# Kernel optimization log

Hardware: AMD Instinct MI355X
Metric: run time of the kernel (lower is better)

The kernel has to match this reference:

```python
import jax, jax.numpy as jnp
import numpy as np

N, K, D = 32768, 1024, 256
TAU = 1.0          # gumbel-softmax temperature (torch default)
KL_WEIGHT = 1.0    # settings.kl_weight stand-in
EPS = 1e-6


def setup_inputs() -> dict:
    key = jax.random.key(0)
    k1, k2, k3 = jax.random.split(key, 3)
    latents = jax.random.normal(k1, (N, D), dtype=jnp.float32)
    # torch init: uniform_(-1/num_protos, 1/num_protos)
    prototypes = jax.random.uniform(k2, (K, D), dtype=jnp.float32,
                                    minval=-1.0 / K, maxval=1.0 / K)
    u = jax.random.uniform(k3, (N, K), dtype=jnp.float32,
                           minval=1e-10, maxval=1.0)
    gumbel = -jnp.log(-jnp.log(u))  # Gumbel(0,1) noise
    return {"latents": latents, "prototypes": prototypes, "gumbel": gumbel}


def reference(latents, prototypes, gumbel):
    # squared euclidean distances latents[:,None,:] - prototypes -> [N, K]
    # expanded form (same math, avoids [N,K,D] intermediate):
    d2 = (jnp.sum(latents * latents, axis=-1, keepdims=True)
          - 2.0 * latents @ prototypes.T
          + jnp.sum(prototypes * prototypes, axis=-1))
    logits = (-d2 + gumbel) / TAU
    logprobs = jax.nn.log_softmax(logits, axis=-1)      # [N, K]
    y_soft = jnp.exp(logprobs)
    # hard=True straight-through one-hot
    idx = jnp.argmax(y_soft, axis=-1)
    y_hard = jax.nn.one_hot(idx, K, dtype=y_soft.dtype)
    onehot = y_hard - jax.lax.stop_gradient(y_soft) + y_soft
    quantized = onehot @ prototypes                     # [N, D]

    # prior over codes (batch mean of probs), broadcast to all rows
    prior = jnp.mean(y_soft + EPS, axis=0)              # [K]
    # KLDivLoss(reduction='batchmean')(logprobs, prior):
    # mean over rows of sum_k prior_k * (log prior_k - logprobs_k)
    capacity = jnp.mean(jnp.sum(prior * (jnp.log(prior) - logprobs), axis=-1))
    ent = -jnp.sum(prior * jnp.log(prior))
    # settings.epoch <= 5000 branch: subtract entropy term
    vq_loss = KL_WEIGHT * capacity - 0.001 * ent
    return quantized, vq_loss
```

## Files before the change

### kernel.cpp

```cpp
#include <hip/hip_runtime.h>
#include <hip/hip_bf16.h>
#include <stdint.h>

#define NN 32768
#define KK 1024
#define DD 256
#define BM 32
#define CHUNK 128
#define NCHUNK (KK / CHUNK)
#define NTHR 512

#define LXS 0
#define LPS 16384
#define LSS (LPS + 65536)
#define LRM (LSS + 65536)
#define LRI (LRM + 128)
#define LTOT (LRI + 128)


typedef __attribute__((ext_vector_type(8))) short bf16x8;
typedef __attribute__((ext_vector_type(4))) float f32x4;

__device__ __forceinline__ uint32_t pkbf2(float a, float b) {
    uint32_t ua = __builtin_bit_cast(uint32_t, a);
    uint32_t ub = __builtin_bit_cast(uint32_t, b);
    ua = (ua + 0x7fffu + ((ua >> 16) & 1u)) >> 16;
    ub = (ub + 0x7fffu + ((ub >> 16) & 1u)) >> 16;
    return ua | (ub << 16);
}
__device__ __forceinline__ float ubf(uint32_t h) {
    return __builtin_bit_cast(float, h << 16);
}

__global__ void vq_init(const float* __restrict__ protos, float* __restrict__ ws) {
    int t = threadIdx.x;
    for (int i = 0; i < 4; ++i) {
        int k = t + i * 256;
        const float4* p4 = reinterpret_cast<const float4*>(protos + (size_t)k * DD);
        float s = 0.f;
#pragma unroll 8
        for (int j = 0; j < DD / 4; ++j) {
            float4 v = p4[j];
            s = fmaf(v.x, v.x, s); s = fmaf(v.y, v.y, s);
            s = fmaf(v.z, v.z, s); s = fmaf(v.w, v.w, s);
        }
        ws[k] = s;
        ws[KK + k] = 0.f;
        ws[2 * KK + k] = 0.f;
    }
}

__global__ void vq_cvt(const float* __restrict__ protos, uint32_t* __restrict__ pb) {
    int idx = blockIdx.x * 256 + threadIdx.x;
    const float4* s = reinterpret_cast<const float4*>(protos + (size_t)idx * 8);
    float4 a = s[0], b = s[1];
    uint4 v;
    v.x = pkbf2(a.x, a.y); v.y = pkbf2(a.z, a.w);
    v.z = pkbf2(b.x, b.y); v.w = pkbf2(b.z, b.w);
    reinterpret_cast<uint4*>(pb)[idx] = v;
}

template<bool PRE>
__global__ __launch_bounds__(NTHR) void vq_mainT(const float* __restrict__ latents,
                                                 const float* __restrict__ protos,
                                                 const float* __restrict__ gumbel,
                                                 float* __restrict__ ws,
                                                 float* __restrict__ out) {
    __shared__ __align__(16) unsigned char sm[LTOT];
    const int t = threadIdx.x;
    const int lane = t & 63;
    const int w = t >> 6;
    const int n0 = blockIdx.x * BM;
    const float* np2 = ws;
    float* colsum_y = ws + KK;
    float* colsum_lp = ws + 2 * KK;
    const uint4* pb = reinterpret_cast<const uint4*>(ws + 3 * KK);

    {
        int row = t >> 4;
        int g0 = (t & 15) * 2;
#pragma unroll
        for (int j = 0; j < 2; ++j) {
            int g = g0 + j;
            const float4* src = reinterpret_cast<const float4*>(
                latents + (size_t)(n0 + row) * DD + g * 8);
            float4 a = src[0], b = src[1];
            uint4 v; v.x = pkbf2(a.x, a.y); v.y = pkbf2(a.z, a.w);
            v.z = pkbf2(b.x, b.y); v.w = pkbf2(b.z, b.w);
            *reinterpret_cast<uint4*>(sm + LXS + row * 512 + ((g ^ (row & 7)) << 4)) = v;
        }
    }

    const int l15 = lane & 15;
    const int l4 = lane >> 4;
    const int pr = w * 16 + l15;

    for (int c = 0; c < NCHUNK; ++c) {
        __syncthreads();
        if (PRE) {
#pragma unroll
            for (int i = 0; i < 8; ++i) {
                int G = t + NTHR * i;
                int p = G >> 5, g = G & 31;
                uint4 v = pb[(size_t)(c * CHUNK + p) * 32 + g];
                *reinterpret_cast<uint4*>(sm + LPS + p * 512 + ((g ^ (p & 7)) << 4)) = v;
            }
        } else {
#pragma unroll
            for (int i = 0; i < 8; ++i) {
                int G = t + NTHR * i;
                int p = G >> 5, g = G & 31;
                const float4* src = reinterpret_cast<const float4*>(
                    protos + (size_t)(c * CHUNK + p) * DD + g * 8);
                float4 a = src[0], b = src[1];
                uint4 v; v.x = pkbf2(a.x, a.y); v.y = pkbf2(a.z, a.w);
                v.z = pkbf2(b.x, b.y); v.w = pkbf2(b.z, b.w);
                *reinterpret_cast<uint4*>(sm + LPS + p * 512 + ((g ^ (p & 7)) << 4)) = v;
            }
        }
        __syncthreads();

        const int pg0 = c * CHUNK + w * 16 + l4 * 4;
        float4 q4 = *reinterpret_cast<const float4*>(np2 + pg0);
        float4 g40 = *reinterpret_cast<const float4*>(gumbel + (size_t)(n0 + l15) * KK + pg0);
        float4 g41 = *reinterpret_cast<const float4*>(gumbel + (size_t)(n0 + 16 + l15) * KK + pg0);

        f32x4 acc0 = {0.f, 0.f, 0.f, 0.f}, acc1 = {0.f, 0.f, 0.f, 0.f};
#pragma unroll
        for (int ks = 0; ks < 8; ++ks) {
            int gi = ks * 4 + l4;
            bf16x8 af = *reinterpret_cast<bf16x8*>(sm + LPS + pr * 512 + ((gi ^ (pr & 7)) << 4));
            bf16x8 b0 = *reinterpret_cast<bf16x8*>(sm + LXS + l15 * 512 + ((gi ^ (l15 & 7)) << 4));
            bf16x8 b1 = *reinterpret_cast<bf16x8*>(sm + LXS + (16 + l15) * 512 + ((gi ^ ((16 + l15) & 7)) << 4));
            acc0 = __builtin_amdgcn_mfma_f32_16x16x32_bf16(af, b0, acc0, 0, 0, 0);
            acc1 = __builtin_amdgcn_mfma_f32_16x16x32_bf16(af, b1, acc1, 0, 0, 0);
        }
        const int Gs = pg0 >> 2;
        {
            int xrow = l15;
            uint2 pk;
            pk.x = pkbf2(fmaf(2.f, acc0.x, -q4.x) + g40.x, fmaf(2.f, acc0.y, -q4.y) + g40.y);
            pk.y = pkbf2(fmaf(2.f, acc0.z, -q4.z) + g40.z, fmaf(2.f, acc0.w, -q4.w) + g40.w);
            *reinterpret_cast<uint2*>(sm + LSS + xrow * 2048 + ((Gs ^ ((xrow & 7) << 1)) << 3)) = pk;
        }
        {
            int xrow = 16 + l15;
            uint2 pk;
            pk.x = pkbf2(fmaf(2.f, acc1.x, -q4.x) + g41.x, fmaf(2.f, acc1.y, -q4.y) + g41.y);
            pk.y = pkbf2(fmaf(2.f, acc1.z, -q4.z) + g41.z, fmaf(2.f, acc1.w, -q4.w) + g41.w);
            *reinterpret_cast<uint2*>(sm + LSS + xrow * 2048 + ((Gs ^ ((xrow & 7) << 1)) << 3)) = pk;
        }
    }
    __syncthreads();

    {
        int row = t >> 4, v = t & 15;
        int sw = (row & 7) << 1;
        uint2 d[16];
#pragma unroll
        for (int j = 0; j < 16; ++j) {
            int G = v + 16 * j;
            d[j] = *reinterpret_cast<uint2*>(sm + LSS + row * 2048 + ((G ^ sw) << 3));
        }
        float m = -3.4e38f; int mi = 0;
#pragma unroll
        for (int j = 0; j < 16; ++j) {
            int c0 = (v + 16 * j) * 4;
            float f0 = ubf(d[j].x & 0xffffu), f1 = ubf(d[j].x >> 16);
            float f2 = ubf(d[j].y & 0xffffu), f3 = ubf(d[j].y >> 16);
            if (f0 > m) { m = f0; mi = c0; }
            if (f1 > m) { m = f1; mi = c0 + 1; }
            if (f2 > m) { m = f2; mi = c0 + 2; }
            if (f3 > m) { m = f3; mi = c0 + 3; }
        }
#pragma unroll
        for (int off = 1; off < 16; off <<= 1) {
            float om = __shfl_xor(m, off);
            int oi = __shfl_xor(mi, off);
            if (om > m || (om == m && oi < mi)) { m = om; mi = oi; }
        }
        float se = 0.f;
#pragma unroll
        for (int j = 0; j < 16; ++j) {
            se += __expf(ubf(d[j].x & 0xffffu) - m);
            se += __expf(ubf(d[j].x >> 16) - m);
            se += __expf(ubf(d[j].y & 0xffffu) - m);
            se += __expf(ubf(d[j].y >> 16) - m);
        }
#pragma unroll
        for (int off = 1; off < 16; off <<= 1) se += __shfl_xor(se, off);
        if (v == 0) {
            *reinterpret_cast<float*>(sm + LRM + row * 4) = m + __logf(se);
            *reinterpret_cast<int*>(sm + LRI + row * 4) = mi;
        }
    }
    __syncthreads();

#pragma unroll
    for (int h = 0; h < 2; ++h) {
        int col = t + h * NTHR;
        int G = col >> 2;
        int e2 = (col & 3) << 1;
        float sy = 0.f, slp = 0.f;
#pragma unroll 8
        for (int r = 0; r < BM; ++r) {
            uint32_t hv = *reinterpret_cast<uint16_t*>(
                sm + LSS + r * 2048 + ((G ^ ((r & 7) << 1)) << 3) + e2);
            float lz = *reinterpret_cast<float*>(sm + LRM + r * 4);
            float lp = ubf(hv) - lz;
            slp += lp;
            sy += __expf(lp);
        }
        atomicAdd(&colsum_y[col], sy);
        atomicAdd(&colsum_lp[col], slp);
    }

    {
        int row = t >> 4, v = t & 15;
        int idx = *reinterpret_cast<int*>(sm + LRI + row * 4);
        const float4* src = reinterpret_cast<const float4*>(protos + (size_t)idx * DD + v * 16);
        float4* dst = reinterpret_cast<float4*>(out + (size_t)(n0 + row) * DD + v * 16);
#pragma unroll
        for (int j = 0; j < 4; ++j) dst[j] = src[j];
    }
}

__global__ void vq_final(const float* __restrict__ ws,
                         float* __restrict__ out, int out_size) {
    __shared__ float part[4];
    int t = threadIdx.x;
    const float invN = 1.0f / (float)NN;
    float a = 0.f;
    for (int j = 0; j < 4; ++j) {
        int k = t + j * 256;
        float prior = fmaf(ws[KK + k], invN, 1e-6f);
        float Lk = ws[2 * KK + k] * invN;
        a += prior * (1.001f * __logf(prior) - Lk);
    }
#pragma unroll
    for (int off = 32; off >= 1; off >>= 1) a += __shfl_xor(a, off);
    if ((t & 63) == 0) part[t >> 6] = a;
    __syncthreads();
    if (t == 0) {
        out[out_size - 1] = part[0] + part[1] + part[2] + part[3];
    }
}

extern "C" void kernel_launch(void* const* d_in, const int* in_sizes, int n_in,
                              void* d_out, int out_size, void* d_ws, size_t ws_size,
                              hipStream_t stream) {
    (void)in_sizes; (void)n_in;
    const float* latents = (const float*)d_in[0];
    const float* protos  = (const float*)d_in[1];
    const float* gumbel  = (const float*)d_in[2];
    float* out           = (float*)d_out;
    float* ws            = (float*)d_ws;

    bool pre = ws_size >= (size_t)(3 * KK * 4 + KK * DD * 2);

    vq_init<<<dim3(1), dim3(256), 0, stream>>>(protos, ws);
    if (pre) {
        vq_cvt<<<dim3(KK * DD / 2048), dim3(256), 0, stream>>>(
            protos, (uint32_t*)(ws + 3 * KK));
        vq_mainT<true><<<dim3(NN / BM), dim3(NTHR), 0, stream>>>(
            latents, protos, gumbel, ws, out);
    } else {
        vq_mainT<false><<<dim3(NN / BM), dim3(NTHR), 0, stream>>>(
            latents, protos, gumbel, ws, out);
    }
    vq_final<<<dim3(1), dim3(256), 0, stream>>>(ws, out, out_size);
}
```

Baseline: 141.9 us.

## Keep score tile in registers and shrink LDS to raise occupancy

The bf16 score tile (32 rows x 1024 codes) now stays in 32 packed registers per thread instead of a 64 KB shared-memory buffer. Row max, argmax, logsumexp and column sums are built from register values with shuffles and small LDS scratch arrays. LDS per block drops from about 146 KB to 80 KB, and launch bounds ask for more resident blocks, so more work can overlap. vq_init also spreads over 4 blocks. The cost is more register pressure, extra barriers and shuffles, and 8x more atomics (per-wave partial column sums).

Measured after the change: 232.2 us. +63.6%, slower.

```diff
diff --git a/kernel.cpp b/kernel.cpp
--- a/kernel.cpp
+++ b/kernel.cpp
@@ -12,10 +12,12 @@
 
 #define LXS 0
 #define LPS 16384
-#define LSS (LPS + 65536)
-#define LRM (LSS + 65536)
-#define LRI (LRM + 128)
-#define LTOT (LRI + 128)
+#define LTOT 81920
+#define SC_MAXP 0
+#define SC_M    2048
+#define SC_MI   2176
+#define SC_ZP   2304
+#define SC_LZ   3328
 
 
 typedef __attribute__((ext_vector_type(8))) short bf16x8;
@@ -33,21 +35,18 @@
 }
 
 __global__ void vq_init(const float* __restrict__ protos, float* __restrict__ ws) {
-    int t = threadIdx.x;
-    for (int i = 0; i < 4; ++i) {
-        int k = t + i * 256;
-        const float4* p4 = reinterpret_cast<const float4*>(protos + (size_t)k * DD);
-        float s = 0.f;
+    int k = blockIdx.x * 256 + threadIdx.x;
+    const float4* p4 = reinterpret_cast<const float4*>(protos + (size_t)k * DD);
+    float s = 0.f;
 #pragma unroll 8
-        for (int j = 0; j < DD / 4; ++j) {
-            float4 v = p4[j];
-            s = fmaf(v.x, v.x, s); s = fmaf(v.y, v.y, s);
-            s = fmaf(v.z, v.z, s); s = fmaf(v.w, v.w, s);
-        }
-        ws[k] = s;
-        ws[KK + k] = 0.f;
-        ws[2 * KK + k] = 0.f;
-    }
+    for (int j = 0; j < DD / 4; ++j) {
+        float4 v = p4[j];
+        s = fmaf(v.x, v.x, s); s = fmaf(v.y, v.y, s);
+        s = fmaf(v.z, v.z, s); s = fmaf(v.w, v.w, s);
+    }
+    ws[k] = s;
+    ws[KK + k] = 0.f;
+    ws[2 * KK + k] = 0.f;
 }
 
 __global__ void vq_cvt(const float* __restrict__ protos, uint32_t* __restrict__ pb) {
@@ -61,16 +60,18 @@
 }
 
 template<bool PRE>
-__global__ __launch_bounds__(NTHR) void vq_mainT(const float* __restrict__ latents,
-                                                 const float* __restrict__ protos,
-                                                 const float* __restrict__ gumbel,
-                                                 float* __restrict__ ws,
-                                                 float* __restrict__ out) {
+__global__ __launch_bounds__(NTHR, 4) void vq_mainT(const float* __restrict__ latents,
+                                                    const float* __restrict__ protos,
+                                                    const float* __restrict__ gumbel,
+                                                    float* __restrict__ ws,
+                                                    float* __restrict__ out) {
     __shared__ __align__(16) unsigned char sm[LTOT];
     const int t = threadIdx.x;
     const int lane = t & 63;
     const int w = t >> 6;
     const int n0 = blockIdx.x * BM;
+    const int l15 = lane & 15;
+    const int l4 = lane >> 4;
     const float* np2 = ws;
     float* colsum_y = ws + KK;
     float* colsum_lp = ws + 2 * KK;
@@ -91,10 +92,11 @@
         }
     }
 
-    const int l15 = lane & 15;
-    const int l4 = lane >> 4;
     const int pr = w * 16 + l15;
-
+    const int cwbase = w * 16 + l4 * 4;
+    uint32_t Sp[32];
+
+#pragma unroll
     for (int c = 0; c < NCHUNK; ++c) {
         __syncthreads();
         if (PRE) {
@@ -120,7 +122,7 @@
         }
         __syncthreads();
 
-        const int pg0 = c * CHUNK + w * 16 + l4 * 4;
+        const int pg0 = c * CHUNK + cwbase;
         float4 q4 = *reinterpret_cast<const float4*>(np2 + pg0);
         float4 g40 = *reinterpret_cast<const float4*>(gumbel + (size_t)(n0 + l15) * KK + pg0);
         float4 g41 = *reinterpret_cast<const float4*>(gumbel + (size_t)(n0 + 16 + l15) * KK + pg0);
@@ -135,89 +137,118 @@
             acc0 = __builtin_amdgcn_mfma_f32_16x16x32_bf16(af, b0, acc0, 0, 0, 0);
             acc1 = __builtin_amdgcn_mfma_f32_16x16x32_bf16(af, b1, acc1, 0, 0, 0);
         }
-        const int Gs = pg0 >> 2;
-        {
-            int xrow = l15;
-            uint2 pk;
-            pk.x = pkbf2(fmaf(2.f, acc0.x, -q4.x) + g40.x, fmaf(2.f, acc0.y, -q4.y) + g40.y);
-            pk.y = pkbf2(fmaf(2.f, acc0.z, -q4.z) + g40.z, fmaf(2.f, acc0.w, -q4.w) + g40.w);
-            *reinterpret_cast<uint2*>(sm + LSS + xrow * 2048 + ((Gs ^ ((xrow & 7) << 1)) << 3)) = pk;
-        }
-        {
-            int xrow = 16 + l15;
-            uint2 pk;
-            pk.x = pkbf2(fmaf(2.f, acc1.x, -q4.x) + g41.x, fmaf(2.f, acc1.y, -q4.y) + g41.y);
-            pk.y = pkbf2(fmaf(2.f, acc1.z, -q4.z) + g41.z, fmaf(2.f, acc1.w, -q4.w) + g41.w);
-            *reinterpret_cast<uint2*>(sm + LSS + xrow * 2048 + ((Gs ^ ((xrow & 7) << 1)) << 3)) = pk;
-        }
-    }
-    __syncthreads();
+        Sp[c * 4 + 0] = pkbf2(fmaf(2.f, acc0.x, -q4.x) + g40.x,
+                              fmaf(2.f, acc0.y, -q4.y) + g40.y);
+        Sp[c * 4 + 1] = pkbf2(fmaf(2.f, acc0.z, -q4.z) + g40.z,
+                              fmaf(2.f, acc0.w, -q4.w) + g40.w);
+        Sp[c * 4 + 2] = pkbf2(fmaf(2.f, acc1.x, -q4.x) + g41.x,
+                              fmaf(2.f, acc1.y, -q4.y) + g41.y);
+        Sp[c * 4 + 3] = pkbf2(fmaf(2.f, acc1.z, -q4.z) + g41.z,
+                              fmaf(2.f, acc1.w, -q4.w) + g41.w);
+    }
+    __syncthreads();
+
+    float m0 = -3.4e38f, m1 = -3.4e38f; int mi0 = 0, mi1 = 0;
+#pragma unroll
+    for (int c = 0; c < NCHUNK; ++c) {
+        int cb = c * CHUNK + cwbase;
+        float f;
+        f = ubf(Sp[c*4+0] & 0xffffu); if (f > m0) { m0 = f; mi0 = cb; }
+        f = ubf(Sp[c*4+0] >> 16);     if (f > m0) { m0 = f; mi0 = cb + 1; }
+        f = ubf(Sp[c*4+1] & 0xffffu); if (f > m0) { m0 = f; mi0 = cb + 2; }
+        f = ubf(Sp[c*4+1] >> 16);     if (f > m0) { m0 = f; mi0 = cb + 3; }
+        f = ubf(Sp[c*4+2] & 0xffffu); if (f > m1) { m1 = f; mi1 = cb; }
+        f = ubf(Sp[c*4+2] >> 16);     if (f > m1) { m1 = f; mi1 = cb + 1; }
+        f = ubf(Sp[c*4+3] & 0xffffu); if (f > m1) { m1 = f; mi1 = cb + 2; }
+        f = ubf(Sp[c*4+3] >> 16);     if (f > m1) { m1 = f; mi1 = cb + 3; }
+    }
+#pragma unroll
+    for (int off = 16; off <= 32; off <<= 1) {
+        float o0 = __shfl_xor(m0, off); int i0 = __shfl_xor(mi0, off);
+        if (o0 > m0 || (o0 == m0 && i0 < mi0)) { m0 = o0; mi0 = i0; }
+        float o1 = __shfl_xor(m1, off); int i1 = __shfl_xor(mi1, off);
+        if (o1 > m1 || (o1 == m1 && i1 < mi1)) { m1 = o1; mi1 = i1; }
+    }
+    if (lane < 16) {
+        *reinterpret_cast<float*>(sm + SC_MAXP + (l15 * 8 + w) * 8) = m0;
+        *reinterpret_cast<int*>(sm + SC_MAXP + (l15 * 8 + w) * 8 + 4) = mi0;
+        *reinterpret_cast<float*>(sm + SC_MAXP + ((16 + l15) * 8 + w) * 8) = m1;
+        *reinterpret_cast<int*>(sm + SC_MAXP + ((16 + l15) * 8 + w) * 8 + 4) = mi1;
+    }
+    __syncthreads();
+    if (t < 32) {
+        float m = -3.4e38f; int mi = 0;
+#pragma unroll
+        for (int j = 0; j < 8; ++j) {
+            float om = *reinterpret_cast<float*>(sm + SC_MAXP + (t * 8 + j) * 8);
+            int oi = *reinterpret_cast<int*>(sm + SC_MAXP + (t * 8 + j) * 8 + 4);
+            if (om > m || (om == m && oi < mi)) { m = om; mi = oi; }
+        }
+        *reinterpret_cast<float*>(sm + SC_M + t * 4) = m;
+        *reinterpret_cast<int*>(sm + SC_MI + t * 4) = mi;
+    }
+    __syncthreads();
+    {
+        float mA = *reinterpret_cast<float*>(sm + SC_M + l15 * 4);
+        float mB = *reinterpret_cast<float*>(sm + SC_M + (16 + l15) * 4);
+        float z0 = 0.f, z1 = 0.f;
+#pragma unroll
+        for (int c = 0; c < NCHUNK; ++c) {
+            z0 += __expf(ubf(Sp[c*4+0] & 0xffffu) - mA) + __expf(ubf(Sp[c*4+0] >> 16) - mA)
+                + __expf(ubf(Sp[c*4+1] & 0xffffu) - mA) + __expf(ubf(Sp[c*4+1] >> 16) - mA);
+            z1 += __expf(ubf(Sp[c*4+2] & 0xffffu) - mB) + __expf(ubf(Sp[c*4+2] >> 16) - mB)
+                + __expf(ubf(Sp[c*4+3] & 0xffffu) - mB) + __expf(ubf(Sp[c*4+3] >> 16) - mB);
+        }
+        z0 += __shfl_xor(z0, 16); z0 += __shfl_xor(z0, 32);
+        z1 += __shfl_xor(z1, 16); z1 += __shfl_xor(z1, 32);
+        if (lane < 16) {
+            *reinterpret_cast<float*>(sm + SC_ZP + (l15 * 8 + w) * 4) = z0;
+            *reinterpret_cast<float*>(sm + SC_ZP + ((16 + l15) * 8 + w) * 4) = z1;
+        }
+    }
+    __syncthreads();
+    if (t < 32) {
+        float Z = 0.f;
+#pragma unroll
+        for (int j = 0; j < 8; ++j)
+            Z += *reinterpret_cast<float*>(sm + SC_ZP + (t * 8 + j) * 4);
+        *reinterpret_cast<float*>(sm + SC_LZ + t * 4) =
+            *reinterpret_cast<float*>(sm + SC_M + t * 4) + __logf(Z);
+    }
+    __syncthreads();
+
+    {
+        float lzA = *reinterpret_cast<float*>(sm + SC_LZ + l15 * 4);
+        float lzB = *reinterpret_cast<float*>(sm + SC_LZ + (16 + l15) * 4);
+#pragma unroll
+        for (int c = 0; c < NCHUNK; ++c) {
+            float a0 = ubf(Sp[c*4+0] & 0xffffu) - lzA, a1 = ubf(Sp[c*4+0] >> 16) - lzA;
+            float a2 = ubf(Sp[c*4+1] & 0xffffu) - lzA, a3 = ubf(Sp[c*4+1] >> 16) - lzA;
+            float b0 = ubf(Sp[c*4+2] & 0xffffu) - lzB, b1 = ubf(Sp[c*4+2] >> 16) - lzB;
+            float b2 = ubf(Sp[c*4+3] & 0xffffu) - lzB, b3 = ubf(Sp[c*4+3] >> 16) - lzB;
+            float sy0 = __expf(a0) + __expf(b0), sy1 = __expf(a1) + __expf(b1);
+            float sy2 = __expf(a2) + __expf(b2), sy3 = __expf(a3) + __expf(b3);
+            float sl0 = a0 + b0, sl1 = a1 + b1, sl2 = a2 + b2, sl3 = a3 + b3;
+#pragma unroll
+            for (int off = 1; off < 16; off <<= 1) {
+                sy0 += __shfl_xor(sy0, off); sy1 += __shfl_xor(sy1, off);
+                sy2 += __shfl_xor(sy2, off); sy3 += __shfl_xor(sy3, off);
+                sl0 += __shfl_xor(sl0, off); sl1 += __shfl_xor(sl1, off);
+                sl2 += __shfl_xor(sl2, off); sl3 += __shfl_xor(sl3, off);
+            }
+            if (l15 == 0) {
+                int cb = c * CHUNK + cwbase;
+                atomicAdd(&colsum_y[cb],     sy0); atomicAdd(&colsum_y[cb + 1], sy1);
+                atomicAdd(&colsum_y[cb + 2], sy2); atomicAdd(&colsum_y[cb + 3], sy3);
+                atomicAdd(&colsum_lp[cb],     sl0); atomicAdd(&colsum_lp[cb + 1], sl1);
+                atomicAdd(&colsum_lp[cb + 2], sl2); atomicAdd(&colsum_lp[cb + 3], sl3);
+            }
+        }
+    }
 
     {
         int row = t >> 4, v = t & 15;
-        int sw = (row & 7) << 1;
-        uint2 d[16];
-#pragma unroll
-        for (int j = 0; j < 16; ++j) {
-            int G = v + 16 * j;
-            d[j] = *reinterpret_cast<uint2*>(sm + LSS + row * 2048 + ((G ^ sw) << 3));
-        }
-        float m = -3.4e38f; int mi = 0;
-#pragma unroll
-        for (int j = 0; j < 16; ++j) {
-            int c0 = (v + 16 * j) * 4;
-            float f0 = ubf(d[j].x & 0xffffu), f1 = ubf(d[j].x >> 16);
-            float f2 = ubf(d[j].y & 0xffffu), f3 = ubf(d[j].y >> 16);
-            if (f0 > m) { m = f0; mi = c0; }
-            if (f1 > m) { m = f1; mi = c0 + 1; }
-            if (f2 > m) { m = f2; mi = c0 + 2; }
-            if (f3 > m) { m = f3; mi = c0 + 3; }
-        }
-#pragma unroll
-        for (int off = 1; off < 16; off <<= 1) {
-            float om = __shfl_xor(m, off);
-            int oi = __shfl_xor(mi, off);
-            if (om > m || (om == m && oi < mi)) { m = om; mi = oi; }
-        }
-        float se = 0.f;
-#pragma unroll
-        for (int j = 0; j < 16; ++j) {
-            se += __expf(ubf(d[j].x & 0xffffu) - m);
-            se += __expf(ubf(d[j].x >> 16) - m);
-            se += __expf(ubf(d[j].y & 0xffffu) - m);
-            se += __expf(ubf(d[j].y >> 16) - m);
-        }
-#pragma unroll
-        for (int off = 1; off < 16; off <<= 1) se += __shfl_xor(se, off);
-        if (v == 0) {
-            *reinterpret_cast<float*>(sm + LRM + row * 4) = m + __logf(se);
-            *reinterpret_cast<int*>(sm + LRI + row * 4) = mi;
-        }
-    }
-    __syncthreads();
-
-#pragma unroll
-    for (int h = 0; h < 2; ++h) {
-        int col = t + h * NTHR;
-        int G = col >> 2;
-        int e2 = (col & 3) << 1;
-        float sy = 0.f, slp = 0.f;
-#pragma unroll 8
-        for (int r = 0; r < BM; ++r) {
-            uint32_t hv = *reinterpret_cast<uint16_t*>(
-                sm + LSS + r * 2048 + ((G ^ ((r & 7) << 1)) << 3) + e2);
-            float lz = *reinterpret_cast<float*>(sm + LRM + r * 4);
-            float lp = ubf(hv) - lz;
-            slp += lp;
-            sy += __expf(lp);
-        }
-        atomicAdd(&colsum_y[col], sy);
-        atomicAdd(&colsum_lp[col], slp);
-    }
-
-    {
-        int row = t >> 4, v = t & 15;
-        int idx = *reinterpret_cast<int*>(sm + LRI + row * 4);
+        int idx = *reinterpret_cast<int*>(sm + SC_MI + row * 4);
         const float4* src = reinterpret_cast<const float4*>(protos + (size_t)idx * DD + v * 16);
         float4* dst = reinterpret_cast<float4*>(out + (size_t)(n0 + row) * DD + v * 16);
 #pragma unroll
@@ -258,7 +289,7 @@
 
     bool pre = ws_size >= (size_t)(3 * KK * 4 + KK * DD * 2);
 
-    vq_init<<<dim3(1), dim3(256), 0, stream>>>(protos, ws);
+    vq_init<<<dim3(4), dim3(256), 0, stream>>>(protos, ws);
     if (pre) {
         vq_cvt<<<dim3(KK * DD / 2048), dim3(256), 0, stream>>>(
             protos, (uint32_t*)(ws + 3 * KK));
```

## Fuse softmax stats into GEMM loop, stream bf16 prototypes from global, shrink LDS

Applied to the files above, without the earlier changes.

The row tile drops from 32 to 16 rows. In the precomputed path the bf16 prototype fragments are read straight from global/L2 instead of being staged in LDS each chunk, and scores are kept packed in registers. Row max, argmax and the exp-sum are accumulated inside the chunk loop, then reduced across waves through a small LDS scratch. The LDS-resident score matrix is gone, and column sums are built with lane shuffles followed by per-column atomics. The aim is to cut LDS from about 147KB to about 10KB so more blocks fit per CU, and to drop several barriers. The cost is more global traffic for prototypes, twice as many blocks and more atomics, plus the exp-sum no longer subtracting the row max. vq_init is also spread over 4 blocks.

Result: slower. 291.3 us (+105.3%).

```diff
diff --git a/kernel.cpp b/kernel.cpp
--- a/kernel.cpp
+++ b/kernel.cpp
@@ -5,17 +5,18 @@
 #define NN 32768
 #define KK 1024
 #define DD 256
-#define BM 32
+#define BM 16
 #define CHUNK 128
-#define NCHUNK (KK / CHUNK)
+#define NCHUNK 8
 #define NTHR 512
 
 #define LXS 0
-#define LPS 16384
-#define LSS (LPS + 65536)
-#define LRM (LSS + 65536)
-#define LRI (LRM + 128)
-#define LTOT (LRI + 128)
+#define SC_MAXP 8192
+#define SC_ZP   9216
+#define SC_LZ   9728
+#define SC_MI   9792
+#define LSCR_END 10240
+#define LPS 10240
 
 
 typedef __attribute__((ext_vector_type(8))) short bf16x8;
@@ -33,21 +34,18 @@
 }
 
 __global__ void vq_init(const float* __restrict__ protos, float* __restrict__ ws) {
-    int t = threadIdx.x;
-    for (int i = 0; i < 4; ++i) {
-        int k = t + i * 256;
-        const float4* p4 = reinterpret_cast<const float4*>(protos + (size_t)k * DD);
-        float s = 0.f;
+    int k = blockIdx.x * 256 + threadIdx.x;
+    const float4* p4 = reinterpret_cast<const float4*>(protos + (size_t)k * DD);
+    float s = 0.f;
 #pragma unroll 8
-        for (int j = 0; j < DD / 4; ++j) {
-            float4 v = p4[j];
-            s = fmaf(v.x, v.x, s); s = fmaf(v.y, v.y, s);
-            s = fmaf(v.z, v.z, s); s = fmaf(v.w, v.w, s);
-        }
-        ws[k] = s;
-        ws[KK + k] = 0.f;
-        ws[2 * KK + k] = 0.f;
-    }
+    for (int j = 0; j < DD / 4; ++j) {
+        float4 v = p4[j];
+        s = fmaf(v.x, v.x, s); s = fmaf(v.y, v.y, s);
+        s = fmaf(v.z, v.z, s); s = fmaf(v.w, v.w, s);
+    }
+    ws[k] = s;
+    ws[KK + k] = 0.f;
+    ws[2 * KK + k] = 0.f;
 }
 
 __global__ void vq_cvt(const float* __restrict__ protos, uint32_t* __restrict__ pb) {
@@ -66,46 +64,38 @@
                                                  const float* __restrict__ gumbel,
                                                  float* __restrict__ ws,
                                                  float* __restrict__ out) {
-    __shared__ __align__(16) unsigned char sm[LTOT];
+    __shared__ __align__(16) unsigned char sm[PRE ? LSCR_END : (LSCR_END + 65536)];
     const int t = threadIdx.x;
     const int lane = t & 63;
     const int w = t >> 6;
     const int n0 = blockIdx.x * BM;
+    const int l15 = lane & 15;
+    const int l4 = lane >> 4;
     const float* np2 = ws;
     float* colsum_y = ws + KK;
     float* colsum_lp = ws + 2 * KK;
     const uint4* pb = reinterpret_cast<const uint4*>(ws + 3 * KK);
 
     {
-        int row = t >> 4;
-        int g0 = (t & 15) * 2;
-#pragma unroll
-        for (int j = 0; j < 2; ++j) {
-            int g = g0 + j;
-            const float4* src = reinterpret_cast<const float4*>(
-                latents + (size_t)(n0 + row) * DD + g * 8);
-            float4 a = src[0], b = src[1];
-            uint4 v; v.x = pkbf2(a.x, a.y); v.y = pkbf2(a.z, a.w);
-            v.z = pkbf2(b.x, b.y); v.w = pkbf2(b.z, b.w);
-            *reinterpret_cast<uint4*>(sm + LXS + row * 512 + ((g ^ (row & 7)) << 4)) = v;
-        }
-    }
-
-    const int l15 = lane & 15;
-    const int l4 = lane >> 4;
+        int row = t >> 5, g = t & 31;
+        const float4* src = reinterpret_cast<const float4*>(
+            latents + (size_t)(n0 + row) * DD + g * 8);
+        float4 a = src[0], b = src[1];
+        uint4 v; v.x = pkbf2(a.x, a.y); v.y = pkbf2(a.z, a.w);
+        v.z = pkbf2(b.x, b.y); v.w = pkbf2(b.z, b.w);
+        *reinterpret_cast<uint4*>(sm + LXS + row * 512 + ((g ^ (row & 7)) << 4)) = v;
+    }
+    if (PRE) __syncthreads();
+
+    const int cwbase = w * 16 + l4 * 4;
     const int pr = w * 16 + l15;
-
+    uint32_t Sp[16];
+    float z = 0.f, m = -3.4e38f; int mi = 0;
+
+#pragma unroll
     for (int c = 0; c < NCHUNK; ++c) {
-        __syncthreads();
-        if (PRE) {
-#pragma unroll
-            for (int i = 0; i < 8; ++i) {
-                int G = t + NTHR * i;
-                int p = G >> 5, g = G & 31;
-                uint4 v = pb[(size_t)(c * CHUNK + p) * 32 + g];
-                *reinterpret_cast<uint4*>(sm + LPS + p * 512 + ((g ^ (p & 7)) << 4)) = v;
-            }
-        } else {
+        if (!PRE) {
+            __syncthreads();
 #pragma unroll
             for (int i = 0; i < 8; ++i) {
                 int G = t + NTHR * i;
@@ -117,111 +107,104 @@
                 v.z = pkbf2(b.x, b.y); v.w = pkbf2(b.z, b.w);
                 *reinterpret_cast<uint4*>(sm + LPS + p * 512 + ((g ^ (p & 7)) << 4)) = v;
             }
-        }
-        __syncthreads();
-
-        const int pg0 = c * CHUNK + w * 16 + l4 * 4;
+            __syncthreads();
+        }
+        const int pg0 = c * CHUNK + cwbase;
         float4 q4 = *reinterpret_cast<const float4*>(np2 + pg0);
-        float4 g40 = *reinterpret_cast<const float4*>(gumbel + (size_t)(n0 + l15) * KK + pg0);
-        float4 g41 = *reinterpret_cast<const float4*>(gumbel + (size_t)(n0 + 16 + l15) * KK + pg0);
-
-        f32x4 acc0 = {0.f, 0.f, 0.f, 0.f}, acc1 = {0.f, 0.f, 0.f, 0.f};
-#pragma unroll
-        for (int ks = 0; ks < 8; ++ks) {
-            int gi = ks * 4 + l4;
-            bf16x8 af = *reinterpret_cast<bf16x8*>(sm + LPS + pr * 512 + ((gi ^ (pr & 7)) << 4));
-            bf16x8 b0 = *reinterpret_cast<bf16x8*>(sm + LXS + l15 * 512 + ((gi ^ (l15 & 7)) << 4));
-            bf16x8 b1 = *reinterpret_cast<bf16x8*>(sm + LXS + (16 + l15) * 512 + ((gi ^ ((16 + l15) & 7)) << 4));
-            acc0 = __builtin_amdgcn_mfma_f32_16x16x32_bf16(af, b0, acc0, 0, 0, 0);
-            acc1 = __builtin_amdgcn_mfma_f32_16x16x32_bf16(af, b1, acc1, 0, 0, 0);
-        }
-        const int Gs = pg0 >> 2;
-        {
-            int xrow = l15;
-            uint2 pk;
-            pk.x = pkbf2(fmaf(2.f, acc0.x, -q4.x) + g40.x, fmaf(2.f, acc0.y, -q4.y) + g40.y);
-            pk.y = pkbf2(fmaf(2.f, acc0.z, -q4.z) + g40.z, fmaf(2.f, acc0.w, -q4.w) + g40.w);
-            *reinterpret_cast<uint2*>(sm + LSS + xrow * 2048 + ((Gs ^ ((xrow & 7) << 1)) << 3)) = pk;
-        }
-        {
-            int xrow = 16 + l15;
-            uint2 pk;
-            pk.x = pkbf2(fmaf(2.f, acc1.x, -q4.x) + g41.x, fmaf(2.f, acc1.y, -q4.y) + g41.y);
-            pk.y = pkbf2(fmaf(2.f, acc1.z, -q4.z) + g41.z, fmaf(2.f, acc1.w, -q4.w) + g41.w);
-            *reinterpret_cast<uint2*>(sm + LSS + xrow * 2048 + ((Gs ^ ((xrow & 7) << 1)) << 3)) = pk;
-        }
+        float4 g4 = *reinterpret_cast<const float4*>(gumbel + (size_t)(n0 + l15) * KK + pg0);
+
+        f32x4 acc = {0.f, 0.f, 0.f, 0.f};
+        if (PRE) {
+            const uint4* afp = pb + (size_t)(c * CHUNK + pr) * 32;
+#pragma unroll
+            for (int ks = 0; ks < 8; ++ks) {
+                int gi = ks * 4 + l4;
+                bf16x8 af = __builtin_bit_cast(bf16x8, afp[gi]);
+                bf16x8 b0 = *reinterpret_cast<bf16x8*>(
+                    sm + LXS + l15 * 512 + ((gi ^ (l15 & 7)) << 4));
+                acc = __builtin_amdgcn_mfma_f32_16x16x32_bf16(af, b0, acc, 0, 0, 0);
+            }
+        } else {
+#pragma unroll
+            for (int ks = 0; ks < 8; ++ks) {
+                int gi = ks * 4 + l4;
+                bf16x8 af = *reinterpret_cast<bf16x8*>(
+                    sm + LPS + pr * 512 + ((gi ^ (pr & 7)) << 4));
+                bf16x8 b0 = *reinterpret_cast<bf16x8*>(
+                    sm + LXS + l15 * 512 + ((gi ^ (l15 & 7)) << 4));
+                acc = __builtin_amdgcn_mfma_f32_16x16x32_bf16(af, b0, acc, 0, 0, 0);
+            }
+        }
+        float s0 = fmaf(2.f, acc.x, -q4.x) + g4.x;
+        float s1 = fmaf(2.f, acc.y, -q4.y) + g4.y;
+        float s2 = fmaf(2.f, acc.z, -q4.z) + g4.z;
+        float s3 = fmaf(2.f, acc.w, -q4.w) + g4.w;
+        z += __expf(s0) + __expf(s1) + __expf(s2) + __expf(s3);
+        if (s0 > m) { m = s0; mi = pg0; }
+        if (s1 > m) { m = s1; mi = pg0 + 1; }
+        if (s2 > m) { m = s2; mi = pg0 + 2; }
+        if (s3 > m) { m = s3; mi = pg0 + 3; }
+        Sp[c * 2]     = pkbf2(s0, s1);
+        Sp[c * 2 + 1] = pkbf2(s2, s3);
+    }
+
+#pragma unroll
+    for (int off = 16; off <= 32; off <<= 1) {
+        float om = __shfl_xor(m, off); int oi = __shfl_xor(mi, off);
+        if (om > m || (om == m && oi < mi)) { m = om; mi = oi; }
+        z += __shfl_xor(z, off);
+    }
+    if (lane < 16) {
+        *reinterpret_cast<float*>(sm + SC_MAXP + (l15 * 8 + w) * 8) = m;
+        *reinterpret_cast<int*>(sm + SC_MAXP + (l15 * 8 + w) * 8 + 4) = mi;
+        *reinterpret_cast<float*>(sm + SC_ZP + (l15 * 8 + w) * 4) = z;
     }
     __syncthreads();
+    if (t < 16) {
+        float mm = -3.4e38f; int mmi = 0; float Z = 0.f;
+#pragma unroll
+        for (int j = 0; j < 8; ++j) {
+            float om = *reinterpret_cast<float*>(sm + SC_MAXP + (t * 8 + j) * 8);
+            int oi = *reinterpret_cast<int*>(sm + SC_MAXP + (t * 8 + j) * 8 + 4);
+            if (om > mm || (om == mm && oi < mmi)) { mm = om; mmi = oi; }
+            Z += *reinterpret_cast<float*>(sm + SC_ZP + (t * 8 + j) * 4);
+        }
+        *reinterpret_cast<float*>(sm + SC_LZ + t * 4) = __logf(Z);
+        *reinterpret_cast<int*>(sm + SC_MI + t * 4) = mmi;
+    }
+    __syncthreads();
 
     {
-        int row = t >> 4, v = t & 15;
-        int sw = (row & 7) << 1;
-        uint2 d[16];
-#pragma unroll
-        for (int j = 0; j < 16; ++j) {
-            int G = v + 16 * j;
-            d[j] = *reinterpret_cast<uint2*>(sm + LSS + row * 2048 + ((G ^ sw) << 3));
-        }
-        float m = -3.4e38f; int mi = 0;
-#pragma unroll
-        for (int j = 0; j < 16; ++j) {
-            int c0 = (v + 16 * j) * 4;
-            float f0 = ubf(d[j].x & 0xffffu), f1 = ubf(d[j].x >> 16);
-            float f2 = ubf(d[j].y & 0xffffu), f3 = ubf(d[j].y >> 16);
-            if (f0 > m) { m = f0; mi = c0; }
-            if (f1 > m) { m = f1; mi = c0 + 1; }
-            if (f2 > m) { m = f2; mi = c0 + 2; }
-            if (f3 > m) { m = f3; mi = c0 + 3; }
-        }
-#pragma unroll
-        for (int off = 1; off < 16; off <<= 1) {
-            float om = __shfl_xor(m, off);
-            int oi = __shfl_xor(mi, off);
-            if (om > m || (om == m && oi < mi)) { m = om; mi = oi; }
-        }
-        float se = 0.f;
-#pragma unroll
-        for (int j = 0; j < 16; ++j) {
-            se += __expf(ubf(d[j].x & 0xffffu) - m);
-            se += __expf(ubf(d[j].x >> 16) - m);
-            se += __expf(ubf(d[j].y & 0xffffu) - m);
-            se += __expf(ubf(d[j].y >> 16) - m);
-        }
-#pragma unroll
-        for (int off = 1; off < 16; off <<= 1) se += __shfl_xor(se, off);
-        if (v == 0) {
-            *reinterpret_cast<float*>(sm + LRM + row * 4) = m + __logf(se);
-            *reinterpret_cast<int*>(sm + LRI + row * 4) = mi;
-        }
-    }
-    __syncthreads();
-
-#pragma unroll
-    for (int h = 0; h < 2; ++h) {
-        int col = t + h * NTHR;
-        int G = col >> 2;
-        int e2 = (col & 3) << 1;
-        float sy = 0.f, slp = 0.f;
-#pragma unroll 8
-        for (int r = 0; r < BM; ++r) {
-            uint32_t hv = *reinterpret_cast<uint16_t*>(
-                sm + LSS + r * 2048 + ((G ^ ((r & 7) << 1)) << 3) + e2);
-            float lz = *reinterpret_cast<float*>(sm + LRM + r * 4);
-            float lp = ubf(hv) - lz;
-            slp += lp;
-            sy += __expf(lp);
-        }
-        atomicAdd(&colsum_y[col], sy);
-        atomicAdd(&colsum_lp[col], slp);
+        float lz = *reinterpret_cast<float*>(sm + SC_LZ + l15 * 4);
+#pragma unroll
+        for (int c = 0; c < NCHUNK; ++c) {
+            float a0 = ubf(Sp[c*2] & 0xffffu) - lz, a1 = ubf(Sp[c*2] >> 16) - lz;
+            float a2 = ubf(Sp[c*2+1] & 0xffffu) - lz, a3 = ubf(Sp[c*2+1] >> 16) - lz;
+            float y0 = __expf(a0), y1 = __expf(a1), y2 = __expf(a2), y3 = __expf(a3);
+#pragma unroll
+            for (int off = 1; off < 16; off <<= 1) {
+                y0 += __shfl_xor(y0, off); y1 += __shfl_xor(y1, off);
+                y2 += __shfl_xor(y2, off); y3 += __shfl_xor(y3, off);
+                a0 += __shfl_xor(a0, off); a1 += __shfl_xor(a1, off);
+                a2 += __shfl_xor(a2, off); a3 += __shfl_xor(a3, off);
+            }
+            if (l15 == 0) {
+                int cb = c * CHUNK + cwbase;
+                atomicAdd(&colsum_y[cb],     y0); atomicAdd(&colsum_y[cb + 1], y1);
+                atomicAdd(&colsum_y[cb + 2], y2); atomicAdd(&colsum_y[cb + 3], y3);
+                atomicAdd(&colsum_lp[cb],     a0); atomicAdd(&colsum_lp[cb + 1], a1);
+                atomicAdd(&colsum_lp[cb + 2], a2); atomicAdd(&colsum_lp[cb + 3], a3);
+            }
+        }
     }
 
     {
-        int row = t >> 4, v = t & 15;
-        int idx = *reinterpret_cast<int*>(sm + LRI + row * 4);
-        const float4* src = reinterpret_cast<const float4*>(protos + (size_t)idx * DD + v * 16);
-        float4* dst = reinterpret_cast<float4*>(out + (size_t)(n0 + row) * DD + v * 16);
-#pragma unroll
-        for (int j = 0; j < 4; ++j) dst[j] = src[j];
+        int row = t >> 5, v = t & 31;
+        int idx = *reinterpret_cast<int*>(sm + SC_MI + row * 4);
+        const float4* src = reinterpret_cast<const float4*>(protos + (size_t)idx * DD + v * 8);
+        float4* dst = reinterpret_cast<float4*>(out + (size_t)(n0 + row) * DD + v * 8);
+        dst[0] = src[0];
+        dst[1] = src[1];
     }
 }
 
@@ -258,7 +241,7 @@
 
     bool pre = ws_size >= (size_t)(3 * KK * 4 + KK * DD * 2);
 
-    vq_init<<<dim3(1), dim3(256), 0, stream>>>(protos, ws);
+    vq_init<<<dim3(4), dim3(256), 0, stream>>>(protos, ws);
     if (pre) {
         vq_cvt<<<dim3(KK * DD / 2048), dim3(256), 0, stream>>>(
             protos, (uint32_t*)(ws + 3 * KK));
```

## Halve row tile, read bf16 prototypes directly from global and drop LDS staging

Applied to the files above, without the earlier changes.

The row tile drops from 32 to 16 latents per block, doubling the grid, and the LDS footprint shrinks. In the precomputed path, the MFMA A-operand is now loaded straight from the global bf16 prototype buffer (L2-resident) instead of staged through shared memory, which removes two barriers per chunk. The per-row softmax and argmax reductions are adapted to 32 lanes per row, and vq_init is spread over 4 blocks. The trade is that each block now rereads the full prototype matrix from L2 while reusing each prototype fragment for only 16 rows, which doubles total prototype traffic.

Measured after the change: 164.0 us. +15.5%, slower.

```diff
diff --git a/kernel.cpp b/kernel.cpp
--- a/kernel.cpp
+++ b/kernel.cpp
@@ -5,17 +5,19 @@
 #define NN 32768
 #define KK 1024
 #define DD 256
-#define BM 32
+#define BM 16
 #define CHUNK 128
 #define NCHUNK (KK / CHUNK)
 #define NTHR 512
 
 #define LXS 0
-#define LPS 16384
-#define LSS (LPS + 65536)
-#define LRM (LSS + 65536)
-#define LRI (LRM + 128)
-#define LTOT (LRI + 128)
+#define LSS 8192
+#define LRM (LSS + 32768)
+#define LRI (LRM + 64)
+#define LEND (LRI + 64)
+#define LPS 41216
+#define LTOT_PRE  41216
+#define LTOT_NPRE (41216 + 65536)
 
 
 typedef __attribute__((ext_vector_type(8))) short bf16x8;
@@ -33,21 +35,18 @@
 }
 
 __global__ void vq_init(const float* __restrict__ protos, float* __restrict__ ws) {
-    int t = threadIdx.x;
-    for (int i = 0; i < 4; ++i) {
-        int k = t + i * 256;
-        const float4* p4 = reinterpret_cast<const float4*>(protos + (size_t)k * DD);
-        float s = 0.f;
+    int k = blockIdx.x * 256 + threadIdx.x;
+    const float4* p4 = reinterpret_cast<const float4*>(protos + (size_t)k * DD);
+    float s = 0.f;
 #pragma unroll 8
-        for (int j = 0; j < DD / 4; ++j) {
-            float4 v = p4[j];
-            s = fmaf(v.x, v.x, s); s = fmaf(v.y, v.y, s);
-            s = fmaf(v.z, v.z, s); s = fmaf(v.w, v.w, s);
-        }
-        ws[k] = s;
-        ws[KK + k] = 0.f;
-        ws[2 * KK + k] = 0.f;
-    }
+    for (int j = 0; j < DD / 4; ++j) {
+        float4 v = p4[j];
+        s = fmaf(v.x, v.x, s); s = fmaf(v.y, v.y, s);
+        s = fmaf(v.z, v.z, s); s = fmaf(v.w, v.w, s);
+    }
+    ws[k] = s;
+    ws[KK + k] = 0.f;
+    ws[2 * KK + k] = 0.f;
 }
 
 __global__ void vq_cvt(const float* __restrict__ protos, uint32_t* __restrict__ pb) {
@@ -66,46 +65,35 @@
                                                  const float* __restrict__ gumbel,
                                                  float* __restrict__ ws,
                                                  float* __restrict__ out) {
-    __shared__ __align__(16) unsigned char sm[LTOT];
+    __shared__ __align__(16) unsigned char sm[PRE ? LTOT_PRE : LTOT_NPRE];
     const int t = threadIdx.x;
     const int lane = t & 63;
     const int w = t >> 6;
     const int n0 = blockIdx.x * BM;
+    const int l15 = lane & 15;
+    const int l4 = lane >> 4;
     const float* np2 = ws;
     float* colsum_y = ws + KK;
     float* colsum_lp = ws + 2 * KK;
     const uint4* pb = reinterpret_cast<const uint4*>(ws + 3 * KK);
 
     {
-        int row = t >> 4;
-        int g0 = (t & 15) * 2;
-#pragma unroll
-        for (int j = 0; j < 2; ++j) {
-            int g = g0 + j;
-            const float4* src = reinterpret_cast<const float4*>(
-                latents + (size_t)(n0 + row) * DD + g * 8);
-            float4 a = src[0], b = src[1];
-            uint4 v; v.x = pkbf2(a.x, a.y); v.y = pkbf2(a.z, a.w);
-            v.z = pkbf2(b.x, b.y); v.w = pkbf2(b.z, b.w);
-            *reinterpret_cast<uint4*>(sm + LXS + row * 512 + ((g ^ (row & 7)) << 4)) = v;
-        }
-    }
-
-    const int l15 = lane & 15;
-    const int l4 = lane >> 4;
+        int row = t >> 5, g = t & 31;
+        const float4* src = reinterpret_cast<const float4*>(
+            latents + (size_t)(n0 + row) * DD + g * 8);
+        float4 a = src[0], b = src[1];
+        uint4 v; v.x = pkbf2(a.x, a.y); v.y = pkbf2(a.z, a.w);
+        v.z = pkbf2(b.x, b.y); v.w = pkbf2(b.z, b.w);
+        *reinterpret_cast<uint4*>(sm + LXS + row * 512 + ((g ^ (row & 7)) << 4)) = v;
+    }
+    __syncthreads();
+
     const int pr = w * 16 + l15;
+    const int cwbase = w * 16 + l4 * 4;
 
     for (int c = 0; c < NCHUNK; ++c) {
-        __syncthreads();
-        if (PRE) {
-#pragma unroll
-            for (int i = 0; i < 8; ++i) {
-                int G = t + NTHR * i;
-                int p = G >> 5, g = G & 31;
-                uint4 v = pb[(size_t)(c * CHUNK + p) * 32 + g];
-                *reinterpret_cast<uint4*>(sm + LPS + p * 512 + ((g ^ (p & 7)) << 4)) = v;
-            }
-        } else {
+        if (!PRE) {
+            __syncthreads();
 #pragma unroll
             for (int i = 0; i < 8; ++i) {
                 int G = t + NTHR * i;
@@ -117,55 +105,57 @@
                 v.z = pkbf2(b.x, b.y); v.w = pkbf2(b.z, b.w);
                 *reinterpret_cast<uint4*>(sm + LPS + p * 512 + ((g ^ (p & 7)) << 4)) = v;
             }
-        }
-        __syncthreads();
-
-        const int pg0 = c * CHUNK + w * 16 + l4 * 4;
+            __syncthreads();
+        }
+        const int pg0 = c * CHUNK + cwbase;
         float4 q4 = *reinterpret_cast<const float4*>(np2 + pg0);
-        float4 g40 = *reinterpret_cast<const float4*>(gumbel + (size_t)(n0 + l15) * KK + pg0);
-        float4 g41 = *reinterpret_cast<const float4*>(gumbel + (size_t)(n0 + 16 + l15) * KK + pg0);
-
-        f32x4 acc0 = {0.f, 0.f, 0.f, 0.f}, acc1 = {0.f, 0.f, 0.f, 0.f};
-#pragma unroll
-        for (int ks = 0; ks < 8; ++ks) {
-            int gi = ks * 4 + l4;
-            bf16x8 af = *reinterpret_cast<bf16x8*>(sm + LPS + pr * 512 + ((gi ^ (pr & 7)) << 4));
-            bf16x8 b0 = *reinterpret_cast<bf16x8*>(sm + LXS + l15 * 512 + ((gi ^ (l15 & 7)) << 4));
-            bf16x8 b1 = *reinterpret_cast<bf16x8*>(sm + LXS + (16 + l15) * 512 + ((gi ^ ((16 + l15) & 7)) << 4));
-            acc0 = __builtin_amdgcn_mfma_f32_16x16x32_bf16(af, b0, acc0, 0, 0, 0);
-            acc1 = __builtin_amdgcn_mfma_f32_16x16x32_bf16(af, b1, acc1, 0, 0, 0);
-        }
-        const int Gs = pg0 >> 2;
+        float4 g4 = *reinterpret_cast<const float4*>(gumbel + (size_t)(n0 + l15) * KK + pg0);
+
+        f32x4 acc = {0.f, 0.f, 0.f, 0.f};
+        if (PRE) {
+            const uint4* afp = pb + (size_t)(c * CHUNK + pr) * 32;
+#pragma unroll
+            for (int ks = 0; ks < 8; ++ks) {
+                int gi = ks * 4 + l4;
+                bf16x8 af = __builtin_bit_cast(bf16x8, afp[gi]);
+                bf16x8 b0 = *reinterpret_cast<bf16x8*>(
+                    sm + LXS + l15 * 512 + ((gi ^ (l15 & 7)) << 4));
+                acc = __builtin_amdgcn_mfma_f32_16x16x32_bf16(af, b0, acc, 0, 0, 0);
+            }
+        } else {
+#pragma unroll
+            for (int ks = 0; ks < 8; ++ks) {
+                int gi = ks * 4 + l4;
+                bf16x8 af = *reinterpret_cast<bf16x8*>(
+                    sm + LPS + pr * 512 + ((gi ^ (pr & 7)) << 4));
+                bf16x8 b0 = *reinterpret_cast<bf16x8*>(
+                    sm + LXS + l15 * 512 + ((gi ^ (l15 & 7)) << 4));
+                acc = __builtin_amdgcn_mfma_f32_16x16x32_bf16(af, b0, acc, 0, 0, 0);
+            }
+        }
         {
-            int xrow = l15;
+            const int Gs = pg0 >> 2;
             uint2 pk;
-            pk.x = pkbf2(fmaf(2.f, acc0.x, -q4.x) + g40.x, fmaf(2.f, acc0.y, -q4.y) + g40.y);
-            pk.y = pkbf2(fmaf(2.f, acc0.z, -q4.z) + g40.z, fmaf(2.f, acc0.w, -q4.w) + g40.w);
-            *reinterpret_cast<uint2*>(sm + LSS + xrow * 2048 + ((Gs ^ ((xrow & 7) << 1)) << 3)) = pk;
-        }
-        {
-            int xrow = 16 + l15;
-            uint2 pk;
-            pk.x = pkbf2(fmaf(2.f, acc1.x, -q4.x) + g41.x, fmaf(2.f, acc1.y, -q4.y) + g41.y);
-            pk.y = pkbf2(fmaf(2.f, acc1.z, -q4.z) + g41.z, fmaf(2.f, acc1.w, -q4.w) + g41.w);
-            *reinterpret_cast<uint2*>(sm + LSS + xrow * 2048 + ((Gs ^ ((xrow & 7) << 1)) << 3)) = pk;
+            pk.x = pkbf2(fmaf(2.f, acc.x, -q4.x) + g4.x, fmaf(2.f, acc.y, -q4.y) + g4.y);
+            pk.y = pkbf2(fmaf(2.f, acc.z, -q4.z) + g4.z, fmaf(2.f, acc.w, -q4.w) + g4.w);
+            *reinterpret_cast<uint2*>(sm + LSS + l15 * 2048 + ((Gs ^ ((l15 & 7) << 1)) << 3)) = pk;
         }
     }
     __syncthreads();
 
     {
-        int row = t >> 4, v = t & 15;
+        int row = t >> 5, v = t & 31;
         int sw = (row & 7) << 1;
-        uint2 d[16];
-#pragma unroll
-        for (int j = 0; j < 16; ++j) {
-            int G = v + 16 * j;
+        uint2 d[8];
+#pragma unroll
+        for (int j = 0; j < 8; ++j) {
+            int G = v + 32 * j;
             d[j] = *reinterpret_cast<uint2*>(sm + LSS + row * 2048 + ((G ^ sw) << 3));
         }
         float m = -3.4e38f; int mi = 0;
 #pragma unroll
-        for (int j = 0; j < 16; ++j) {
-            int c0 = (v + 16 * j) * 4;
+        for (int j = 0; j < 8; ++j) {
+            int c0 = (v + 32 * j) * 4;
             float f0 = ubf(d[j].x & 0xffffu), f1 = ubf(d[j].x >> 16);
             float f2 = ubf(d[j].y & 0xffffu), f3 = ubf(d[j].y >> 16);
             if (f0 > m) { m = f0; mi = c0; }
@@ -174,21 +164,21 @@
             if (f3 > m) { m = f3; mi = c0 + 3; }
         }
 #pragma unroll
-        for (int off = 1; off < 16; off <<= 1) {
+        for (int off = 1; off < 32; off <<= 1) {
             float om = __shfl_xor(m, off);
             int oi = __shfl_xor(mi, off);
             if (om > m || (om == m && oi < mi)) { m = om; mi = oi; }
         }
         float se = 0.f;
 #pragma unroll
-        for (int j = 0; j < 16; ++j) {
+        for (int j = 0; j < 8; ++j) {
             se += __expf(ubf(d[j].x & 0xffffu) - m);
             se += __expf(ubf(d[j].x >> 16) - m);
             se += __expf(ubf(d[j].y & 0xffffu) - m);
             se += __expf(ubf(d[j].y >> 16) - m);
         }
 #pragma unroll
-        for (int off = 1; off < 16; off <<= 1) se += __shfl_xor(se, off);
+        for (int off = 1; off < 32; off <<= 1) se += __shfl_xor(se, off);
         if (v == 0) {
             *reinterpret_cast<float*>(sm + LRM + row * 4) = m + __logf(se);
             *reinterpret_cast<int*>(sm + LRI + row * 4) = mi;
@@ -216,12 +206,12 @@
     }
 
     {
-        int row = t >> 4, v = t & 15;
+        int row = t >> 5, v = t & 31;
         int idx = *reinterpret_cast<int*>(sm + LRI + row * 4);
-        const float4* src = reinterpret_cast<const float4*>(protos + (size_t)idx * DD + v * 16);
-        float4* dst = reinterpret_cast<float4*>(out + (size_t)(n0 + row) * DD + v * 16);
-#pragma unroll
-        for (int j = 0; j < 4; ++j) dst[j] = src[j];
+        const float4* src = reinterpret_cast<const float4*>(protos + (size_t)idx * DD + v * 8);
+        float4* dst = reinterpret_cast<float4*>(out + (size_t)(n0 + row) * DD + v * 8);
+        dst[0] = src[0];
+        dst[1] = src[1];
     }
 }
 
@@ -258,7 +248,7 @@
 
     bool pre = ws_size >= (size_t)(3 * KK * 4 + KK * DD * 2);
 
-    vq_init<<<dim3(1), dim3(256), 0, stream>>>(protos, ws);
+    vq_init<<<dim3(4), dim3(256), 0, stream>>>(protos, ws);
     if (pre) {
         vq_cvt<<<dim3(KK * DD / 2048), dim3(256), 0, stream>>>(
             protos, (uint32_t*)(ws + 3 * KK));
```
